# Performance work log

Hardware: AMD Instinct MI355X
Metric: run time of the kernel (lower is better)

## Reference

```python
import jax, jax.numpy as jnp
import numpy as np

H, W = 4096, 4096
KH, KW = 11, 11


def setup_inputs() -> dict:
    key = jax.random.key(0)
    k1, k2 = jax.random.split(key)
    x = jax.random.normal(k1, (H, W), dtype=jnp.float32)
    weight = jax.random.uniform(k2, (KH, KW), dtype=jnp.float32)
    bias = jnp.zeros((1,), dtype=jnp.float32)
    return {"x": x, "weight": weight, "bias": bias}


def reference(x, weight, bias):
    # corr2d: valid 2D cross-correlation of a single-channel image with a
    # single kernel, then add scalar bias. Output shape [H-KH+1, W-KW+1].
    out = jax.lax.conv_general_dilated(
        x[None, None, :, :],            # NCHW, N=C=1
        weight[None, None, :, :],       # OIHW, O=I=1
        window_strides=(1, 1),
        padding="VALID",
        dimension_numbers=("NCHW", "OIHW", "NCHW"),
    )[0, 0]
    return out + bias[0]
```

## Files before the change

kernel.cpp:

```cpp
#include <hip/hip_runtime.h>
#include <hip/hip_bf16.h>

#define IH 4096
#define IW 4096
#define KH 11
#define KW 11
#define OH (IH - KH + 1)
#define OW (IW - KW + 1)

#define BM 64
#define BN 64
#define TROWS   74
#define TSTRIDE 84
#define NC4     20
#define NCHUNK  (TROWS * NC4)
#define NITER   6
#define B_OFF   (TROWS * TSTRIDE)

#define TILES_X 64
#define NPAIR   2048

typedef short bf16x4 __attribute__((ext_vector_type(4)));
typedef short bf16x8 __attribute__((ext_vector_type(8)));
typedef float f32x4  __attribute__((ext_vector_type(4)));

__device__ __forceinline__ short f2b(float f) {
    __hip_bfloat16 h = __float2bfloat16(f);
    return __builtin_bit_cast(short, h);
}

__device__ __forceinline__ void stage_load(float4 G[NITER],
                                           const float* __restrict__ x,
                                           int gx0, int gy0, int tid) {
#pragma unroll
    for (int it = 0; it < NITER; ++it) {
        const int i = tid + it * 256;
        float4 v = make_float4(0.f, 0.f, 0.f, 0.f);
        if (i < NCHUNK) {
            const int r  = i / NC4;
            const int c4 = i - r * NC4;
            const int gy = gy0 + r;
            const int gx = gx0 + c4 * 4;
            if (gy < IH && gx + 3 < IW) {
                v = *reinterpret_cast<const float4*>(x + (size_t)gy * IW + gx);
            }
        }
        G[it] = v;
    }
}

__device__ __forceinline__ void stage_write(short* __restrict__ lds,
                                            const float4 G[NITER], int tid) {
#pragma unroll
    for (int it = 0; it < NITER; ++it) {
        const int i = tid + it * 256;
        if (i < NCHUNK) {
            const int r  = i / NC4;
            const int c4 = i - r * NC4;
            bf16x4 b = { f2b(G[it].x), f2b(G[it].y), f2b(G[it].z), f2b(G[it].w) };
            *reinterpret_cast<bf16x4*>(&lds[r * TSTRIDE + c4 * 4]) = b;
        }
    }
}

__device__ __forceinline__ void compute_tile(const short* __restrict__ lds,
                                             float bv, float* __restrict__ out,
                                             int gx0, int gy0,
                                             int wv, int g, int li) {
    f32x4 acc[4] = {};
    const short* ap = &lds[(16 * wv + li) * TSTRIDE + g * 8];
    const short* bp = &lds[B_OFF + li * 32 + g * 8];

#pragma unroll 1
    for (int kh = 0; kh < KH; ++kh) {
        const bf16x8 bfrag = *reinterpret_cast<const bf16x8*>(bp + kh * 512);
#pragma unroll
        for (int c = 0; c < 4; ++c) {
            bf16x4 lo = *reinterpret_cast<const bf16x4*>(ap + c * 16);
            bf16x4 hi = *reinterpret_cast<const bf16x4*>(ap + c * 16 + 4);
            bf16x8 a  = __builtin_shufflevector(lo, hi, 0, 1, 2, 3, 4, 5, 6, 7);
            acc[c] = __builtin_amdgcn_mfma_f32_16x16x32_bf16(a, bfrag, acc[c],
                                                             0, 0, 0);
        }
        ap += TSTRIDE;
    }

#pragma unroll
    for (int c = 0; c < 4; ++c) {
        const int ox = gx0 + c * 16 + li;
        if (ox < OW) {
#pragma unroll
            for (int r = 0; r < 4; ++r) {
                const int oy = gy0 + wv * 16 + g * 4 + r;
                if (oy < OH) {
                    out[(size_t)oy * OW + ox] = acc[c][r] + bv;
                }
            }
        }
    }
}

__global__ __launch_bounds__(256)
void conv2d_mfma2(const float* __restrict__ x,
                  const float* __restrict__ w,
                  const float* __restrict__ bias,
                  float* __restrict__ out) {
    __shared__ short lds[B_OFF + KH * 512];

    const int tid = threadIdx.x;
    const int pair = (blockIdx.x & 7) * (NPAIR / 8) + (blockIdx.x >> 3);
    const int t0 = pair * 2;
    const int gy0   = (t0 >> 6) * BM;
    const int gx0_0 = (t0 & (TILES_X - 1)) * BN;
    const int gx0_1 = gx0_0 + BN;

    const int lane = tid & 63;
    const int wv   = tid >> 6;
    const int g    = lane >> 4;
    const int li   = lane & 15;
    const float bv = bias[0];

    {
        float4 G0[NITER];
        stage_load(G0, x, gx0_0, gy0, tid);
        stage_write(lds, G0, tid);
    }
#pragma unroll
    for (int t = 0; t < 22; ++t) {
        const int idx = tid + t * 256;
        const int kh = idx >> 9;
        const int j  = (idx >> 5) & 15;
        const int k  = idx & 31;
        const int d  = k - j;
        const float val = (d >= 0 && d < KW) ? w[kh * KW + d] : 0.f;
        lds[B_OFF + idx] = f2b(val);
    }
    __syncthreads();

    float4 G[NITER];
    stage_load(G, x, gx0_1, gy0, tid);
    __builtin_amdgcn_sched_barrier(0);

    compute_tile(lds, bv, out, gx0_0, gy0, wv, g, li);

    __syncthreads();
    stage_write(lds, G, tid);
    __syncthreads();

    compute_tile(lds, bv, out, gx0_1, gy0, wv, g, li);
}

extern "C" void kernel_launch(void* const* d_in, const int* in_sizes, int n_in,
                              void* d_out, int out_size, void* d_ws, size_t ws_size,
                              hipStream_t stream) {
    const float* x    = (const float*)d_in[0];
    const float* w    = (const float*)d_in[1];
    const float* bias = (const float*)d_in[2];
    float* out        = (float*)d_out;

    dim3 grid(NPAIR);
    dim3 block(256);
    conv2d_mfma2<<<grid, block, 0, stream>>>(x, w, bias, out);
}
```

Measured before the change: 42.75 us.

## Process four tiles per block with double-buffered LDS pipeline

Each block now handles four horizontally adjacent 64x64 output tiles instead of two, using two LDS tile buffers so the next tile's staging write overlaps less with compute and needs only one barrier per tile. The weight Toeplitz matrix is built once per block and amortized over more tiles. Grid halves to 1024 blocks, which lowers parallelism and wave count on the device and raises LDS use per block, possibly reducing occupancy.

```diff
diff --git a/kernel.cpp b/kernel.cpp
--- a/kernel.cpp
+++ b/kernel.cpp
@@ -15,10 +15,10 @@
 #define NC4     20
 #define NCHUNK  (TROWS * NC4)
 #define NITER   6
-#define B_OFF   (TROWS * TSTRIDE)
+#define TILE_SHORTS (TROWS * TSTRIDE)
 
 #define TILES_X 64
-#define NPAIR   2048
+#define NBLK    1024
 
 typedef short bf16x4 __attribute__((ext_vector_type(4)));
 typedef short bf16x8 __attribute__((ext_vector_type(8)));
@@ -49,7 +49,7 @@
     }
 }
 
-__device__ __forceinline__ void stage_write(short* __restrict__ lds,
+__device__ __forceinline__ void stage_write(short* __restrict__ tb,
                                             const float4 G[NITER], int tid) {
 #pragma unroll
     for (int it = 0; it < NITER; ++it) {
@@ -58,18 +58,19 @@
             const int r  = i / NC4;
             const int c4 = i - r * NC4;
             bf16x4 b = { f2b(G[it].x), f2b(G[it].y), f2b(G[it].z), f2b(G[it].w) };
-            *reinterpret_cast<bf16x4*>(&lds[r * TSTRIDE + c4 * 4]) = b;
+            *reinterpret_cast<bf16x4*>(&tb[r * TSTRIDE + c4 * 4]) = b;
         }
     }
 }
 
-__device__ __forceinline__ void compute_tile(const short* __restrict__ lds,
+__device__ __forceinline__ void compute_tile(const short* __restrict__ tb,
+                                             const short* __restrict__ bmat,
                                              float bv, float* __restrict__ out,
                                              int gx0, int gy0,
                                              int wv, int g, int li) {
     f32x4 acc[4] = {};
-    const short* ap = &lds[(16 * wv + li) * TSTRIDE + g * 8];
-    const short* bp = &lds[B_OFF + li * 32 + g * 8];
+    const short* ap = &tb[(16 * wv + li) * TSTRIDE + g * 8];
+    const short* bp = &bmat[li * 32 + g * 8];
 
 #pragma unroll 1
     for (int kh = 0; kh < KH; ++kh) {
@@ -101,18 +102,18 @@
 }
 
 __global__ __launch_bounds__(256)
-void conv2d_mfma2(const float* __restrict__ x,
+void conv2d_mfma4(const float* __restrict__ x,
                   const float* __restrict__ w,
                   const float* __restrict__ bias,
                   float* __restrict__ out) {
-    __shared__ short lds[B_OFF + KH * 512];
+    __shared__ short buf[2][TILE_SHORTS];
+    __shared__ short bmat[KH * 512];
 
     const int tid = threadIdx.x;
-    const int pair = (blockIdx.x & 7) * (NPAIR / 8) + (blockIdx.x >> 3);
-    const int t0 = pair * 2;
-    const int gy0   = (t0 >> 6) * BM;
-    const int gx0_0 = (t0 & (TILES_X - 1)) * BN;
-    const int gx0_1 = gx0_0 + BN;
+    const int blk = (blockIdx.x & 7) * (NBLK / 8) + (blockIdx.x >> 3);
+    const int t0  = blk * 4;
+    const int gy0 = (t0 >> 6) * BM;
+    const int gxb = (t0 & (TILES_X - 1)) * BN;
 
     const int lane = tid & 63;
     const int wv   = tid >> 6;
@@ -122,8 +123,8 @@
 
     {
         float4 G0[NITER];
-        stage_load(G0, x, gx0_0, gy0, tid);
-        stage_write(lds, G0, tid);
+        stage_load(G0, x, gxb, gy0, tid);
+        stage_write(buf[0], G0, tid);
     }
 #pragma unroll
     for (int t = 0; t < 22; ++t) {
@@ -133,21 +134,23 @@
         const int k  = idx & 31;
         const int d  = k - j;
         const float val = (d >= 0 && d < KW) ? w[kh * KW + d] : 0.f;
-        lds[B_OFF + idx] = f2b(val);
+        bmat[idx] = f2b(val);
     }
     __syncthreads();
 
     float4 G[NITER];
-    stage_load(G, x, gx0_1, gy0, tid);
-    __builtin_amdgcn_sched_barrier(0);
-
-    compute_tile(lds, bv, out, gx0_0, gy0, wv, g, li);
-
-    __syncthreads();
-    stage_write(lds, G, tid);
-    __syncthreads();
-
-    compute_tile(lds, bv, out, gx0_1, gy0, wv, g, li);
+#pragma unroll 1
+    for (int t = 0; t < 4; ++t) {
+        if (t < 3) {
+            stage_load(G, x, gxb + (t + 1) * BN, gy0, tid);
+            __builtin_amdgcn_sched_barrier(0);
+        }
+        compute_tile(buf[t & 1], bmat, bv, out, gxb + t * BN, gy0, wv, g, li);
+        if (t < 3) {
+            stage_write(buf[(t + 1) & 1], G, tid);
+            __syncthreads();
+        }
+    }
 }
 
 extern "C" void kernel_launch(void* const* d_in, const int* in_sizes, int n_in,
@@ -158,7 +161,7 @@
     const float* bias = (const float*)d_in[2];
     float* out        = (float*)d_out;
 
-    dim3 grid(NPAIR);
+    dim3 grid(NBLK);
     dim3 block(256);
-    conv2d_mfma2<<<grid, block, 0, stream>>>(x, w, bias, out);
+    conv2d_mfma4<<<grid, block, 0, stream>>>(x, w, bias, out);
 }
```

Result: faster. 40.94 us (-4.2%).

## Give each wave a private LDS input tile to drop block barriers

Applied to the files above, without the earlier changes.

Each of the four waves now loads and converts its own 26-row haloed slice of the input into a private LDS region, instead of the block sharing one 74-row tile. This removes the two __syncthreads between the first and second tile, so each wave can write its next tile and compute independently. The trade-off is redundant halo loads (26 rows per wave versus about 18.5 shared), more LDS per block, and more staging registers per thread (9 float4 instead of 6).

```diff
diff --git a/kernel.cpp b/kernel.cpp
--- a/kernel.cpp
+++ b/kernel.cpp
@@ -10,12 +10,12 @@
 
 #define BM 64
 #define BN 64
-#define TROWS   74
+#define WROWS   26
 #define TSTRIDE 84
-#define NC4     20
-#define NCHUNK  (TROWS * NC4)
-#define NITER   6
-#define B_OFF   (TROWS * TSTRIDE)
+#define WTILE   (WROWS * TSTRIDE)
+#define NWCHUNK (WROWS * 20)
+#define WNITER  9
+#define B_OFF   (4 * WTILE)
 
 #define TILES_X 64
 #define NPAIR   2048
@@ -29,17 +29,17 @@
     return __builtin_bit_cast(short, h);
 }
 
-__device__ __forceinline__ void stage_load(float4 G[NITER],
+__device__ __forceinline__ void stage_load(float4 G[WNITER],
                                            const float* __restrict__ x,
-                                           int gx0, int gy0, int tid) {
+                                           int gx0, int gy0w, int lane) {
 #pragma unroll
-    for (int it = 0; it < NITER; ++it) {
-        const int i = tid + it * 256;
+    for (int it = 0; it < WNITER; ++it) {
+        const int i = lane + it * 64;
         float4 v = make_float4(0.f, 0.f, 0.f, 0.f);
-        if (i < NCHUNK) {
-            const int r  = i / NC4;
-            const int c4 = i - r * NC4;
-            const int gy = gy0 + r;
+        if (i < NWCHUNK) {
+            const int r  = i / 20;
+            const int c4 = i - r * 20;
+            const int gy = gy0w + r;
             const int gx = gx0 + c4 * 4;
             if (gy < IH && gx + 3 < IW) {
                 v = *reinterpret_cast<const float4*>(x + (size_t)gy * IW + gx);
@@ -49,27 +49,28 @@
     }
 }
 
-__device__ __forceinline__ void stage_write(short* __restrict__ lds,
-                                            const float4 G[NITER], int tid) {
+__device__ __forceinline__ void stage_write(short* __restrict__ wb,
+                                            const float4 G[WNITER], int lane) {
 #pragma unroll
-    for (int it = 0; it < NITER; ++it) {
-        const int i = tid + it * 256;
-        if (i < NCHUNK) {
-            const int r  = i / NC4;
-            const int c4 = i - r * NC4;
+    for (int it = 0; it < WNITER; ++it) {
+        const int i = lane + it * 64;
+        if (i < NWCHUNK) {
+            const int r  = i / 20;
+            const int c4 = i - r * 20;
             bf16x4 b = { f2b(G[it].x), f2b(G[it].y), f2b(G[it].z), f2b(G[it].w) };
-            *reinterpret_cast<bf16x4*>(&lds[r * TSTRIDE + c4 * 4]) = b;
+            *reinterpret_cast<bf16x4*>(&wb[r * TSTRIDE + c4 * 4]) = b;
         }
     }
 }
 
-__device__ __forceinline__ void compute_tile(const short* __restrict__ lds,
+__device__ __forceinline__ void compute_tile(const short* __restrict__ wb,
+                                             const short* __restrict__ bmat,
                                              float bv, float* __restrict__ out,
                                              int gx0, int gy0,
                                              int wv, int g, int li) {
     f32x4 acc[4] = {};
-    const short* ap = &lds[(16 * wv + li) * TSTRIDE + g * 8];
-    const short* bp = &lds[B_OFF + li * 32 + g * 8];
+    const short* ap = &wb[li * TSTRIDE + g * 8];
+    const short* bp = &bmat[li * 32 + g * 8];
 
 #pragma unroll 1
     for (int kh = 0; kh < KH; ++kh) {
@@ -101,30 +102,27 @@
 }
 
 __global__ __launch_bounds__(256)
-void conv2d_mfma2(const float* __restrict__ x,
-                  const float* __restrict__ w,
-                  const float* __restrict__ bias,
-                  float* __restrict__ out) {
+void conv2d_mfma_wp(const float* __restrict__ x,
+                    const float* __restrict__ w,
+                    const float* __restrict__ bias,
+                    float* __restrict__ out) {
     __shared__ short lds[B_OFF + KH * 512];
 
     const int tid = threadIdx.x;
     const int pair = (blockIdx.x & 7) * (NPAIR / 8) + (blockIdx.x >> 3);
-    const int t0 = pair * 2;
-    const int gy0   = (t0 >> 6) * BM;
-    const int gx0_0 = (t0 & (TILES_X - 1)) * BN;
-    const int gx0_1 = gx0_0 + BN;
+    const int t0   = pair * 2;
+    const int gy0  = (t0 >> 6) * BM;
+    const int gxb  = (t0 & (TILES_X - 1)) * BN;
 
     const int lane = tid & 63;
     const int wv   = tid >> 6;
     const int g    = lane >> 4;
     const int li   = lane & 15;
+    const int gy0w = gy0 + 16 * wv;
+    short* wb = &lds[wv * WTILE];
+    const short* bmat = &lds[B_OFF];
     const float bv = bias[0];
 
-    {
-        float4 G0[NITER];
-        stage_load(G0, x, gx0_0, gy0, tid);
-        stage_write(lds, G0, tid);
-    }
 #pragma unroll
     for (int t = 0; t < 22; ++t) {
         const int idx = tid + t * 256;
@@ -135,19 +133,21 @@
         const float val = (d >= 0 && d < KW) ? w[kh * KW + d] : 0.f;
         lds[B_OFF + idx] = f2b(val);
     }
+    {
+        float4 G0[WNITER];
+        stage_load(G0, x, gxb, gy0w, lane);
+        stage_write(wb, G0, lane);
+    }
     __syncthreads();
 
-    float4 G[NITER];
-    stage_load(G, x, gx0_1, gy0, tid);
+    float4 G[WNITER];
+    stage_load(G, x, gxb + BN, gy0w, lane);
     __builtin_amdgcn_sched_barrier(0);
 
-    compute_tile(lds, bv, out, gx0_0, gy0, wv, g, li);
+    compute_tile(wb, bmat, bv, out, gxb, gy0, wv, g, li);
 
-    __syncthreads();
-    stage_write(lds, G, tid);
-    __syncthreads();
-
-    compute_tile(lds, bv, out, gx0_1, gy0, wv, g, li);
+    stage_write(wb, G, lane);
+    compute_tile(wb, bmat, bv, out, gxb + BN, gy0, wv, g, li);
 }
 
 extern "C" void kernel_launch(void* const* d_in, const int* in_sizes, int n_in,
@@ -160,5 +160,5 @@
 
     dim3 grid(NPAIR);
     dim3 block(256);
-    conv2d_mfma2<<<grid, block, 0, stream>>>(x, w, bias, out);
+    conv2d_mfma_wp<<<grid, block, 0, stream>>>(x, w, bias, out);
 }
```

Result: slower. 44.94 us (+5.1%).
